# Performance work log

Hardware: AMD Instinct MI355X
Metric: run time of the kernel (lower is better)

## Reference

```python
import jax, jax.numpy as jnp
import numpy as np

T, B, IN, HID, NL = 256, 256, 64, 512, 2
LS = HID // NL  # per-layer hidden size of GRUCellStack


def setup_inputs() -> dict:
    key = jax.random.key(0)
    ks = jax.random.split(key, 9)
    w = lambda k, shape: (jax.random.normal(k, shape, jnp.float32) * 0.05)
    return {
        "obs": jax.random.normal(ks[0], (T, B, IN), jnp.float32),
        "reset": jax.random.randint(ks[1], (T, B), 0, 2).astype(bool),
        "h": jnp.zeros((B, HID), jnp.float32),
        "W_lin": w(ks[2], (HID, IN)),
        "b_lin": jnp.zeros((HID,), jnp.float32),
        "w_ih0": w(ks[3], (3 * LS, HID)),
        "w_hh0": w(ks[4], (3 * LS, LS)),
        "b_ih0": jnp.zeros((3 * LS,), jnp.float32),
        "b_hh0": jnp.zeros((3 * LS,), jnp.float32),
        "w_ih1": w(ks[5], (3 * LS, LS)),
        "w_hh1": w(ks[6], (3 * LS, LS)),
        "b_ih1": jnp.zeros((3 * LS,), jnp.float32),
        "b_hh1": jnp.zeros((3 * LS,), jnp.float32),
    }


def _gru_cell(i_gates, h, w_hh, b_hh):
    # PyTorch nn.GRUCell math; i_gates = x @ w_ih.T + b_ih precomputed.
    h_gates = h @ w_hh.T + b_hh
    ir, iz, in_ = jnp.split(i_gates, 3, axis=-1)
    hr, hz, hn = jnp.split(h_gates, 3, axis=-1)
    r = jax.nn.sigmoid(ir + hr)
    z = jax.nn.sigmoid(iz + hz)
    n = jnp.tanh(in_ + r * hn)
    return (1.0 - z) * n + z * h


def reference(obs, reset, h, W_lin, b_lin, w_ih0, w_hh0, b_ih0, b_hh0,
              w_ih1, w_hh1, b_ih1, b_hh1):
    # embed all timesteps at once: [T,B,HID]
    x = obs.astype(jnp.float32) @ W_lin.T + b_lin
    # layer-0 input-side gates depend only on x -> precompute: [T,B,3*LS]
    ig0 = x @ w_ih0.T + b_ih0
    mask = (~reset).astype(jnp.float32)[..., None]  # [T,B,1]

    def step(hc, inp):
        ig0_t, m_t = inp
        hc = hc * m_t                      # reset masking of full stacked state
        h0, h1 = jnp.split(hc, 2, axis=-1)  # per-layer states [B,LS]
        h0n = _gru_cell(ig0_t, h0, w_hh0, b_hh0)
        ig1 = h0n @ w_ih1.T + b_ih1
        h1n = _gru_cell(ig1, h1, w_hh1, b_hh1)
        hn = jnp.concatenate([h0n, h1n], axis=-1)  # [B,HID]
        return hn, hn

    _, states_h = jax.lax.scan(step, h, (ig0, mask))
    return states_h  # [T,B,HID]
```

## Files before the change

### kernel.cpp

```cpp
#include <hip/hip_runtime.h>

#define T_    256
#define B_    256
#define IN_   64
#define HID_  512
#define LS_   256
#define G3_   768
#define TBS_  16
#define MBT_  128
#define WP_   264
#define FSTRIDE_ 128

typedef short bf16x8v __attribute__((ext_vector_type(8)));
typedef float f32x4  __attribute__((ext_vector_type(4)));
typedef unsigned long long u64;

#define MFMA_B16(A, B, C) __builtin_amdgcn_mfma_f32_16x16x32_bf16(A, B, C, 0, 0, 0)

__device__ __forceinline__ unsigned short f2bf(float f) {
  union { float f; unsigned u; } v; v.f = f;
  unsigned r = v.u + 0x7fffu + ((v.u >> 16) & 1u);
  return (unsigned short)(r >> 16);
}
__device__ __forceinline__ float sigm(float x) { return 1.0f / (1.0f + __expf(-x)); }
__device__ __forceinline__ float tanh_f(float x) {
  x = fminf(fmaxf(x, -15.0f), 15.0f);
  float e = __expf(-2.0f * x);
  return (1.0f - e) / (1.0f + e);
}

__device__ __forceinline__ void st2_coh(unsigned short* p, unsigned short v) {
  __hip_atomic_store(p, v, __ATOMIC_RELAXED, __HIP_MEMORY_SCOPE_AGENT);
}
__device__ __forceinline__ bf16x8v ld16_coh(const unsigned short* p) {
  union { u64 q[2]; bf16x8v v; } u;
  u.q[0] = __hip_atomic_load((const u64*)p,     __ATOMIC_RELAXED, __HIP_MEMORY_SCOPE_AGENT);
  u.q[1] = __hip_atomic_load((const u64*)(p+4), __ATOMIC_RELAXED, __HIP_MEMORY_SCOPE_AGENT);
  return u.v;
}

__global__ void prep_all(const float* __restrict__ whh0, const float* __restrict__ wih1,
                         const float* __restrict__ whh1, const unsigned char* __restrict__ rst,
                         const float* __restrict__ W_lin, const float* __restrict__ b_lin,
                         const float* __restrict__ w_ih0, const float* __restrict__ b_ih0,
                         unsigned short* __restrict__ dst, unsigned short* __restrict__ wc,
                         float* __restrict__ bc, int* __restrict__ flagp,
                         int* __restrict__ flags) {
  const int bx = blockIdx.x;
  const int tid = threadIdx.x;
  if (bx < 1152) {
    const int idx = bx * 512 + tid;
    const int N1 = G3_ * LS_;
    if (idx < 3 * N1) {
      float v;
      if (idx < N1)            v = whh0[idx];
      else if (idx < 2 * N1)   v = wih1[idx - N1];
      else                     v = whh1[idx - 2 * N1];
      dst[idx] = f2bf(v);
    }
    if (bx == 1 && tid < 32) flags[tid * FSTRIDE_] = 0;
    if (bx == 0) {
      __shared__ int f;
      if (tid == 0) f = 0;
      __syncthreads();
      int any = 0;
      for (int i = 0; i < 8; ++i) {
        int off = tid * 8 + i;
        if ((off & 3) && rst[off]) any = 1;
      }
      if (any) atomicOr(&f, 1);
      __syncthreads();
      if (tid == 0) *flagp = f;
    }
  } else {
    const int n = (bx - 1152) * 8 + (tid >> 6);
    const int i = tid & 63;
    const float* wrow = w_ih0 + (size_t)n * HID_;
    float acc = 0.f;
    for (int h = 0; h < HID_; ++h) acc += wrow[h] * W_lin[h * IN_ + i];
    wc[n * IN_ + i] = f2bf(acc);
    float pb = 0.f;
    for (int h = i; h < HID_; h += 64) pb += wrow[h] * b_lin[h];
#pragma unroll
    for (int off = 32; off > 0; off >>= 1) pb += __shfl_down(pb, off);
    if (i == 0) bc[n] = pb + b_ih0[n];
  }
}

__global__ __launch_bounds__(512, 2) void gru_main(
    const float* __restrict__ obs, const unsigned char* __restrict__ rst,
    const float* __restrict__ h_init,
    const unsigned short* __restrict__ wc,
    const unsigned short* __restrict__ whh0g,
    const unsigned short* __restrict__ wih1g, const unsigned short* __restrict__ whh1g,
    const float* __restrict__ bcp, const float* __restrict__ bhh0,
    const float* __restrict__ bih1, const float* __restrict__ bhh1,
    const int* __restrict__ flagp, int* __restrict__ flag0,
    unsigned short* __restrict__ hx0, unsigned short* __restrict__ hx1,
    float* __restrict__ out) {

  __shared__ __align__(16) unsigned short wlds[3 * 96 * WP_];
  __shared__ int s_sm[128];
  __shared__ int s_start_sh;

  const int tid  = threadIdx.x;
  const int lane = tid & 63;
  const int w    = tid >> 6;
  const int l15  = lane & 15;
  const int quad = lane >> 4;

  const int x  = blockIdx.x;
  const int cx = x & 7, m8 = x >> 3;
  const int j  = m8 & 7;
  const int team = cx * 4 + (m8 >> 3);
  const int bg = team & 1, tc = team >> 1;
  const int b0 = bg * MBT_, t0 = tc * TBS_;

  int* f0 = flag0 + team * FSTRIDE_;

  const int flag = *flagp;
#define RVAL(i) (rst[flag ? (i) : ((i) << 2)] != 0)

#pragma unroll
  for (int q = 0; q < 3; ++q) {
    const unsigned short* src = (q == 0) ? whh0g : (q == 1) ? wih1g : whh1g;
    for (int cid = tid; cid < 96 * 32; cid += 512) {
      int lr = cid >> 5, off8 = (cid & 31) * 8;
      int g = lr >> 5, cc = lr & 31;
      int grow = (g << 8) + (j << 5) + cc;
      *(f32x4*)&wlds[(q * 96 + lr) * WP_ + off8] =
          *(const f32x4*)&src[(size_t)grow * 256 + off8];
    }
  }

  float b0r[2], b0z[2], b0i[2], b0h[2], b1r[2], b1z[2], b1i[2], b1h[2];
#pragma unroll
  for (int cg = 0; cg < 2; ++cg) {
    const int c = j * 32 + cg * 16 + l15;
    b0r[cg] = bcp[c] + bhh0[c];
    b0z[cg] = bcp[256 + c] + bhh0[256 + c];
    b0i[cg] = bcp[512 + c];
    b0h[cg] = bhh0[512 + c];
    b1r[cg] = bih1[c] + bhh1[c];
    b1z[cg] = bih1[256 + c] + bhh1[256 + c];
    b1i[cg] = bih1[512 + c];
    b1h[cg] = bhh1[512 + c];
  }

  if (tid < 128) {
    int s = 0;
    for (int tt = t0; tt >= 1; --tt) {
      if (RVAL(tt * B_ + b0 + tid)) { s = tt; break; }
    }
    s_sm[tid] = s;
  }
  __syncthreads();
  if (tid == 0) {
    int s = s_sm[0];
    for (int k = 1; k < 128; ++k) s = s < s_sm[k] ? s : s_sm[k];
    s_start_sh = s;
  }
  __syncthreads();
  const int s_start = s_start_sh;

  bf16x8v h0A[8], h1A[8];
  const bf16x8v z8 = {0, 0, 0, 0, 0, 0, 0, 0};
#pragma unroll
  for (int kc = 0; kc < 8; ++kc) { h0A[kc] = z8; h1A[kc] = z8; }
  float h0v[2][4] = {{0.f}}, h1v[2][4] = {{0.f}};
#pragma unroll
  for (int cg = 0; cg < 2; ++cg)
#pragma unroll
    for (int r = 0; r < 4; ++r) { h0v[cg][r] = 0.f; h1v[cg][r] = 0.f; }
  if (s_start == 0) {
    const float* hrow = h_init + (size_t)(b0 + w * 16 + l15) * HID_;
#pragma unroll
    for (int kc = 0; kc < 8; ++kc) {
      f32x4 u0 = *(const f32x4*)(hrow + kc * 32 + quad * 8);
      f32x4 u1 = *(const f32x4*)(hrow + kc * 32 + quad * 8 + 4);
      f32x4 v0 = *(const f32x4*)(hrow + 256 + kc * 32 + quad * 8);
      f32x4 v1 = *(const f32x4*)(hrow + 256 + kc * 32 + quad * 8 + 4);
      bf16x8v a, b;
#pragma unroll
      for (int e = 0; e < 4; ++e) {
        a[e] = (short)f2bf(u0[e]); a[4 + e] = (short)f2bf(u1[e]);
        b[e] = (short)f2bf(v0[e]); b[4 + e] = (short)f2bf(v1[e]);
      }
      h0A[kc] = a; h1A[kc] = b;
    }
#pragma unroll
    for (int cg = 0; cg < 2; ++cg)
#pragma unroll
      for (int r = 0; r < 4; ++r) {
        const int m = w * 16 + quad * 4 + r;
        const int c = j * 32 + cg * 16 + l15;
        h0v[cg][r] = h_init[(size_t)(b0 + m) * HID_ + c];
        h1v[cg][r] = h_init[(size_t)(b0 + m) * HID_ + 256 + c];
      }
  }

  const unsigned short* wR0 = &wlds[(0 * 96 + 0 * 32 + l15) * WP_];
  const unsigned short* wZ0 = &wlds[(0 * 96 + 1 * 32 + l15) * WP_];
  const unsigned short* wN0 = &wlds[(0 * 96 + 2 * 32 + l15) * WP_];
  const unsigned short* iR1 = &wlds[(1 * 96 + 0 * 32 + l15) * WP_];
  const unsigned short* iZ1 = &wlds[(1 * 96 + 1 * 32 + l15) * WP_];
  const unsigned short* iN1 = &wlds[(1 * 96 + 2 * 32 + l15) * WP_];
  const unsigned short* hR1 = &wlds[(2 * 96 + 0 * 32 + l15) * WP_];
  const unsigned short* hZ1 = &wlds[(2 * 96 + 1 * 32 + l15) * WP_];
  const unsigned short* hN1 = &wlds[(2 * 96 + 2 * 32 + l15) * WP_];
#define CGO_ (16 * WP_)

  f32x4 ou0a, ou0b, ou1a, ou1b;
  {
    const float* po = obs + ((size_t)s_start * B_ + b0 + w * 16 + l15) * IN_;
    ou0a = __builtin_nontemporal_load((const f32x4*)(po + quad * 8));
    ou0b = __builtin_nontemporal_load((const f32x4*)(po + quad * 8 + 4));
    ou1a = __builtin_nontemporal_load((const f32x4*)(po + 32 + quad * 8));
    ou1b = __builtin_nontemporal_load((const f32x4*)(po + 32 + quad * 8 + 4));
  }

  for (int t = s_start; t < t0 + TBS_; ++t) {
    const int  kk = t - s_start + 1;
    const bool wr = (t >= t0);
    const bool rs0 = RVAL(t * B_ + b0 + w * 16 + l15);
    bool rse[4];
#pragma unroll
    for (int r = 0; r < 4; ++r) rse[r] = RVAL(t * B_ + b0 + w * 16 + quad * 4 + r);

    f32x4 ar[2], az[2], ani[2], anh[2];
#pragma unroll
    for (int cg = 0; cg < 2; ++cg) {
      ar[cg] = (f32x4){0.f, 0.f, 0.f, 0.f};
      az[cg] = ar[cg]; ani[cg] = ar[cg]; anh[cg] = ar[cg];
    }
    {
#pragma unroll
      for (int kc = 0; kc < 2; ++kc) {
        f32x4 u0 = kc ? ou1a : ou0a;
        f32x4 u1 = kc ? ou1b : ou0b;
        bf16x8v oA;
#pragma unroll
        for (int e = 0; e < 4; ++e) { oA[e] = (short)f2bf(u0[e]); oA[4 + e] = (short)f2bf(u1[e]); }
#pragma unroll
        for (int cg = 0; cg < 2; ++cg) {
          const size_t wo = (size_t)(j * 32 + cg * 16 + l15) * 64 + kc * 32 + quad * 8;
          bf16x8v br = *(const bf16x8v*)&wc[wo];
          bf16x8v bz = *(const bf16x8v*)&wc[wo + (size_t)256 * 64];
          bf16x8v bn = *(const bf16x8v*)&wc[wo + (size_t)512 * 64];
          ar[cg]  = MFMA_B16(oA, br, ar[cg]);
          az[cg]  = MFMA_B16(oA, bz, az[cg]);
          ani[cg] = MFMA_B16(oA, bn, ani[cg]);
        }
      }
    }
#pragma unroll
    for (int kc = 0; kc < 8; ++kc) {
      bf16x8v am = rs0 ? z8 : h0A[kc];
      const int o = kc * 32 + quad * 8;
#pragma unroll
      for (int cg = 0; cg < 2; ++cg) {
        ar[cg]  = MFMA_B16(am, *(const bf16x8v*)&wR0[o + cg * CGO_], ar[cg]);
        az[cg]  = MFMA_B16(am, *(const bf16x8v*)&wZ0[o + cg * CGO_], az[cg]);
        anh[cg] = MFMA_B16(am, *(const bf16x8v*)&wN0[o + cg * CGO_], anh[cg]);
      }
    }
    {
      unsigned short* hw = hx0 + ((size_t)team * 2 + (kk & 1)) * (MBT_ * 256);
#pragma unroll
      for (int cg = 0; cg < 2; ++cg)
#pragma unroll
        for (int r = 0; r < 4; ++r) {
          const int m = w * 16 + quad * 4 + r;
          float rr = sigm(ar[cg][r] + b0r[cg]);
          float zz = sigm(az[cg][r] + b0z[cg]);
          float nn = tanh_f(ani[cg][r] + b0i[cg] + rr * (anh[cg][r] + b0h[cg]));
          float hp = rse[r] ? 0.f : h0v[cg][r];
          float hv = (1.f - zz) * nn + zz * hp;
          h0v[cg][r] = hv;
          st2_coh(hw + m * 256 + j * 32 + cg * 16 + l15, f2bf(hv));
        }
    }
    __syncthreads();
    if (tid == 0) {
      __hip_atomic_fetch_add(f0, 1, __ATOMIC_RELAXED, __HIP_MEMORY_SCOPE_AGENT);
      int cap = 0;
      while (__hip_atomic_load(f0, __ATOMIC_RELAXED, __HIP_MEMORY_SCOPE_AGENT)
                 < 8 * kk && cap < (1 << 16)) { __builtin_amdgcn_s_sleep(2); ++cap; }
    }
    __syncthreads();
    {
      const unsigned short* hr0 =
          hx0 + ((size_t)team * 2 + (kk & 1)) * (MBT_ * 256) + (w * 16 + l15) * 256;
#pragma unroll
      for (int kc = 0; kc < 8; ++kc)
        h0A[kc] = ld16_coh(hr0 + kc * 32 + quad * 8);
      if (kk >= 2) {
        const unsigned short* hr1 =
            hx1 + ((size_t)team * 2 + ((kk - 1) & 1)) * (MBT_ * 256) + (w * 16 + l15) * 256;
#pragma unroll
        for (int kc = 0; kc < 8; ++kc)
          h1A[kc] = ld16_coh(hr1 + kc * 32 + quad * 8);
      }
    }
    if (wr) {
#pragma unroll
      for (int cg = 0; cg < 2; ++cg)
#pragma unroll
        for (int r = 0; r < 4; ++r) {
          const int m = w * 16 + quad * 4 + r;
          __builtin_nontemporal_store(h0v[cg][r],
              &out[((size_t)t * B_ + b0 + m) * HID_ + j * 32 + cg * 16 + l15]);
        }
    }
    if (t - 1 >= t0) {
#pragma unroll
      for (int cg = 0; cg < 2; ++cg)
#pragma unroll
        for (int r = 0; r < 4; ++r) {
          const int m = w * 16 + quad * 4 + r;
          __builtin_nontemporal_store(h1v[cg][r],
              &out[((size_t)(t - 1) * B_ + b0 + m) * HID_ + 256 + j * 32 + cg * 16 + l15]);
        }
    }
    {
      const int tn = (t + 1 < t0 + TBS_) ? t + 1 : t;
      const float* po = obs + ((size_t)tn * B_ + b0 + w * 16 + l15) * IN_;
      ou0a = __builtin_nontemporal_load((const f32x4*)(po + quad * 8));
      ou0b = __builtin_nontemporal_load((const f32x4*)(po + quad * 8 + 4));
      ou1a = __builtin_nontemporal_load((const f32x4*)(po + 32 + quad * 8));
      ou1b = __builtin_nontemporal_load((const f32x4*)(po + 32 + quad * 8 + 4));
    }

#pragma unroll
    for (int cg = 0; cg < 2; ++cg) {
      ar[cg] = (f32x4){0.f, 0.f, 0.f, 0.f};
      az[cg] = ar[cg]; ani[cg] = ar[cg]; anh[cg] = ar[cg];
    }
#pragma unroll
    for (int kc = 0; kc < 8; ++kc) {
      bf16x8v ai_ = h0A[kc];
      bf16x8v am  = rs0 ? z8 : h1A[kc];
      const int o = kc * 32 + quad * 8;
#pragma unroll
      for (int cg = 0; cg < 2; ++cg) {
        ar[cg]  = MFMA_B16(ai_, *(const bf16x8v*)&iR1[o + cg * CGO_], ar[cg]);
        az[cg]  = MFMA_B16(ai_, *(const bf16x8v*)&iZ1[o + cg * CGO_], az[cg]);
        ani[cg] = MFMA_B16(ai_, *(const bf16x8v*)&iN1[o + cg * CGO_], ani[cg]);
        ar[cg]  = MFMA_B16(am, *(const bf16x8v*)&hR1[o + cg * CGO_], ar[cg]);
        az[cg]  = MFMA_B16(am, *(const bf16x8v*)&hZ1[o + cg * CGO_], az[cg]);
        anh[cg] = MFMA_B16(am, *(const bf16x8v*)&hN1[o + cg * CGO_], anh[cg]);
      }
    }
    {
      unsigned short* hw = hx1 + ((size_t)team * 2 + (kk & 1)) * (MBT_ * 256);
#pragma unroll
      for (int cg = 0; cg < 2; ++cg)
#pragma unroll
        for (int r = 0; r < 4; ++r) {
          const int m = w * 16 + quad * 4 + r;
          float rr = sigm(ar[cg][r] + b1r[cg]);
          float zz = sigm(az[cg][r] + b1z[cg]);
          float nn = tanh_f(ani[cg][r] + b1i[cg] + rr * (anh[cg][r] + b1h[cg]));
          float hp = rse[r] ? 0.f : h1v[cg][r];
          float hv = (1.f - zz) * nn + zz * hp;
          h1v[cg][r] = hv;
          st2_coh(hw + m * 256 + j * 32 + cg * 16 + l15, f2bf(hv));
        }
    }
  }
  {
    const int tl = t0 + TBS_ - 1;
#pragma unroll
    for (int cg = 0; cg < 2; ++cg)
#pragma unroll
      for (int r = 0; r < 4; ++r) {
        const int m = w * 16 + quad * 4 + r;
        __builtin_nontemporal_store(h1v[cg][r],
            &out[((size_t)tl * B_ + b0 + m) * HID_ + 256 + j * 32 + cg * 16 + l15]);
      }
  }
#undef RVAL
#undef CGO_
}

extern "C" void kernel_launch(void* const* d_in, const int* in_sizes, int n_in,
                              void* d_out, int out_size, void* d_ws, size_t ws_size,
                              hipStream_t stream) {
  const float* obs    = (const float*)d_in[0];
  const unsigned char* rst = (const unsigned char*)d_in[1];
  const float* h_init = (const float*)d_in[2];
  const float* W_lin  = (const float*)d_in[3];
  const float* b_lin  = (const float*)d_in[4];
  const float* w_ih0  = (const float*)d_in[5];
  const float* w_hh0  = (const float*)d_in[6];
  const float* b_ih0  = (const float*)d_in[7];
  const float* b_hh0  = (const float*)d_in[8];
  const float* w_ih1  = (const float*)d_in[9];
  const float* w_hh1  = (const float*)d_in[10];
  const float* b_ih1  = (const float*)d_in[11];
  const float* b_hh1  = (const float*)d_in[12];

  char* w = (char*)d_ws;
  unsigned short* wcp   = (unsigned short*)(w);
  unsigned short* whh0b = (unsigned short*)(w + 98304);
  unsigned short* wih1b = (unsigned short*)(w + 491520);
  unsigned short* whh1b = (unsigned short*)(w + 884736);
  float*          bcp   = (float*)(w + 1277952);
  int*            flagp = (int*)(w + 1281024);
  int*            flags = (int*)(w + 1281088);
  unsigned short* hx0   = (unsigned short*)(w + 1310720);
  unsigned short* hx1   = (unsigned short*)(w + 1310720 + 4194304);

  prep_all<<<1152 + 96, 512, 0, stream>>>(w_hh0, w_ih1, w_hh1, rst,
                                          W_lin, b_lin, w_ih0, b_ih0,
                                          whh0b, wcp, bcp, flagp, flags);
  gru_main<<<256, 512, 0, stream>>>(obs, rst, h_init, wcp, whh0b, wih1b, whh1b,
                                    bcp, b_hh0, b_ih1, b_hh1, flagp,
                                    flags, hx0, hx1, (float*)d_out);
}
```

Baseline: 655.4 us.

## Permute K dimension so hidden-state exchange uses packed fragment-ordered stores and loads

Reorders the K index of the recurrent weights in LDS and of the exchanged hidden-state buffers, so each lane stores two bf16 values as one 32-bit atomic instead of two 16-bit stores. The exchange buffer is laid out in MFMA-fragment order so the coherent reloads by each lane hit contiguous 512-byte spans across the wave. The goal is to halve the number of coherent global stores and make the per-step cross-block state exchange better coalesced. The cost is more complex index arithmetic and a K permutation that must stay consistent between the weights, the initial state and the exchanged state.

New measurement: 705.0 us. +7.6%, slower.

```diff
diff --git a/kernel.cpp b/kernel.cpp
--- a/kernel.cpp
+++ b/kernel.cpp
@@ -29,14 +29,18 @@
   return (1.0f - e) / (1.0f + e);
 }
 
-__device__ __forceinline__ void st2_coh(unsigned short* p, unsigned short v) {
-  __hip_atomic_store(p, v, __ATOMIC_RELAXED, __HIP_MEMORY_SCOPE_AGENT);
-}
-__device__ __forceinline__ bf16x8v ld16_coh(const unsigned short* p) {
+__device__ __forceinline__ bf16x8v ld_frag_coh(const char* tb, int w8kc, int l15, int quad) {
+  const char* p = tb + ((size_t)w8kc << 10) + (size_t)((((quad << 4) + l15)) << 3);
   union { u64 q[2]; bf16x8v v; } u;
-  u.q[0] = __hip_atomic_load((const u64*)p,     __ATOMIC_RELAXED, __HIP_MEMORY_SCOPE_AGENT);
-  u.q[1] = __hip_atomic_load((const u64*)(p+4), __ATOMIC_RELAXED, __HIP_MEMORY_SCOPE_AGENT);
+  u.q[0] = __hip_atomic_load((const u64*)p,         __ATOMIC_RELAXED, __HIP_MEMORY_SCOPE_AGENT);
+  u.q[1] = __hip_atomic_load((const u64*)(p + 512), __ATOMIC_RELAXED, __HIP_MEMORY_SCOPE_AGENT);
   return u.v;
+}
+__device__ __forceinline__ void st_pair_coh(char* tb, int m, int j, int l15, unsigned pack) {
+  const int p0 = l15 << 1;
+  char* p = tb + ((size_t)((((m >> 4) << 3) + j)) << 10)
+               + (size_t)(((((p0 >> 3) << 4) + (m & 15)) << 3) + ((p0 & 4) << 7) + ((p0 & 3) << 1));
+  __hip_atomic_store((unsigned*)p, pack, __ATOMIC_RELAXED, __HIP_MEMORY_SCOPE_AGENT);
 }
 
 __global__ void prep_all(const float* __restrict__ whh0, const float* __restrict__ wih1,
@@ -125,11 +129,19 @@
   for (int q = 0; q < 3; ++q) {
     const unsigned short* src = (q == 0) ? whh0g : (q == 1) ? wih1g : whh1g;
     for (int cid = tid; cid < 96 * 32; cid += 512) {
-      int lr = cid >> 5, off8 = (cid & 31) * 8;
+      int lr = cid >> 5, ch = cid & 31;
       int g = lr >> 5, cc = lr & 31;
       int grow = (g << 8) + (j << 5) + cc;
-      *(f32x4*)&wlds[(q * 96 + lr) * WP_ + off8] =
-          *(const f32x4*)&src[(size_t)grow * 256 + off8];
+      int kc = ch >> 2, q4 = (ch & 3) << 2;
+      const unsigned short* s = &src[(size_t)grow * 256 + (kc << 5) + q4];
+      u64 A = *(const u64*)s;
+      u64 B = *(const u64*)(s + 16);
+      u64 o0 = (A & 0xffffull) | ((B & 0xffffull) << 16) |
+               (((A >> 16) & 0xffffull) << 32) | (((B >> 16) & 0xffffull) << 48);
+      u64 o1 = ((A >> 32) & 0xffffull) | (((B >> 32) & 0xffffull) << 16) |
+               (((A >> 48) & 0xffffull) << 32) | (((B >> 48) & 0xffffull) << 48);
+      unsigned short* d = &wlds[(q * 96 + lr) * WP_ + (ch << 3)];
+      *(u64*)d = o0; *((u64*)(d + 4)) = o1;
     }
   }
 
@@ -167,7 +179,7 @@
   const bf16x8v z8 = {0, 0, 0, 0, 0, 0, 0, 0};
 #pragma unroll
   for (int kc = 0; kc < 8; ++kc) { h0A[kc] = z8; h1A[kc] = z8; }
-  float h0v[2][4] = {{0.f}}, h1v[2][4] = {{0.f}};
+  float h0v[2][4], h1v[2][4];
 #pragma unroll
   for (int cg = 0; cg < 2; ++cg)
 #pragma unroll
@@ -176,15 +188,13 @@
     const float* hrow = h_init + (size_t)(b0 + w * 16 + l15) * HID_;
 #pragma unroll
     for (int kc = 0; kc < 8; ++kc) {
-      f32x4 u0 = *(const f32x4*)(hrow + kc * 32 + quad * 8);
-      f32x4 u1 = *(const f32x4*)(hrow + kc * 32 + quad * 8 + 4);
-      f32x4 v0 = *(const f32x4*)(hrow + 256 + kc * 32 + quad * 8);
-      f32x4 v1 = *(const f32x4*)(hrow + 256 + kc * 32 + quad * 8 + 4);
       bf16x8v a, b;
 #pragma unroll
-      for (int e = 0; e < 4; ++e) {
-        a[e] = (short)f2bf(u0[e]); a[4 + e] = (short)f2bf(u1[e]);
-        b[e] = (short)f2bf(v0[e]); b[4 + e] = (short)f2bf(v1[e]);
+      for (int e = 0; e < 8; ++e) {
+        const int p  = (quad << 3) + e;
+        const int lk = ((p & 1) << 4) + (p >> 1);
+        a[e] = (short)f2bf(hrow[(kc << 5) + lk]);
+        b[e] = (short)f2bf(hrow[256 + (kc << 5) + lk]);
       }
       h0A[kc] = a; h1A[kc] = b;
     }
@@ -233,24 +243,22 @@
       ar[cg] = (f32x4){0.f, 0.f, 0.f, 0.f};
       az[cg] = ar[cg]; ani[cg] = ar[cg]; anh[cg] = ar[cg];
     }
-    {
-#pragma unroll
-      for (int kc = 0; kc < 2; ++kc) {
-        f32x4 u0 = kc ? ou1a : ou0a;
-        f32x4 u1 = kc ? ou1b : ou0b;
-        bf16x8v oA;
-#pragma unroll
-        for (int e = 0; e < 4; ++e) { oA[e] = (short)f2bf(u0[e]); oA[4 + e] = (short)f2bf(u1[e]); }
-#pragma unroll
-        for (int cg = 0; cg < 2; ++cg) {
-          const size_t wo = (size_t)(j * 32 + cg * 16 + l15) * 64 + kc * 32 + quad * 8;
-          bf16x8v br = *(const bf16x8v*)&wc[wo];
-          bf16x8v bz = *(const bf16x8v*)&wc[wo + (size_t)256 * 64];
-          bf16x8v bn = *(const bf16x8v*)&wc[wo + (size_t)512 * 64];
-          ar[cg]  = MFMA_B16(oA, br, ar[cg]);
-          az[cg]  = MFMA_B16(oA, bz, az[cg]);
-          ani[cg] = MFMA_B16(oA, bn, ani[cg]);
-        }
+#pragma unroll
+    for (int kc = 0; kc < 2; ++kc) {
+      f32x4 u0 = kc ? ou1a : ou0a;
+      f32x4 u1 = kc ? ou1b : ou0b;
+      bf16x8v oA;
+#pragma unroll
+      for (int e = 0; e < 4; ++e) { oA[e] = (short)f2bf(u0[e]); oA[4 + e] = (short)f2bf(u1[e]); }
+#pragma unroll
+      for (int cg = 0; cg < 2; ++cg) {
+        const size_t wo = (size_t)(j * 32 + cg * 16 + l15) * 64 + kc * 32 + quad * 8;
+        bf16x8v br = *(const bf16x8v*)&wc[wo];
+        bf16x8v bz = *(const bf16x8v*)&wc[wo + (size_t)256 * 64];
+        bf16x8v bn = *(const bf16x8v*)&wc[wo + (size_t)512 * 64];
+        ar[cg]  = MFMA_B16(oA, br, ar[cg]);
+        az[cg]  = MFMA_B16(oA, bz, az[cg]);
+        ani[cg] = MFMA_B16(oA, bn, ani[cg]);
       }
     }
 #pragma unroll
@@ -265,20 +273,23 @@
       }
     }
     {
-      unsigned short* hw = hx0 + ((size_t)team * 2 + (kk & 1)) * (MBT_ * 256);
-#pragma unroll
-      for (int cg = 0; cg < 2; ++cg)
-#pragma unroll
-        for (int r = 0; r < 4; ++r) {
-          const int m = w * 16 + quad * 4 + r;
+      char* tbw = (char*)(hx0 + (size_t)(team * 2 + (kk & 1)) * (MBT_ * 256));
+#pragma unroll
+      for (int r = 0; r < 4; ++r) {
+        const int m = w * 16 + quad * 4 + r;
+        float hvv[2];
+#pragma unroll
+        for (int cg = 0; cg < 2; ++cg) {
           float rr = sigm(ar[cg][r] + b0r[cg]);
           float zz = sigm(az[cg][r] + b0z[cg]);
           float nn = tanh_f(ani[cg][r] + b0i[cg] + rr * (anh[cg][r] + b0h[cg]));
           float hp = rse[r] ? 0.f : h0v[cg][r];
-          float hv = (1.f - zz) * nn + zz * hp;
-          h0v[cg][r] = hv;
-          st2_coh(hw + m * 256 + j * 32 + cg * 16 + l15, f2bf(hv));
+          hvv[cg] = (1.f - zz) * nn + zz * hp;
+          h0v[cg][r] = hvv[cg];
         }
+        st_pair_coh(tbw, m, j, l15,
+                    (unsigned)f2bf(hvv[0]) | ((unsigned)f2bf(hvv[1]) << 16));
+      }
     }
     __syncthreads();
     if (tid == 0) {
@@ -289,17 +300,16 @@
     }
     __syncthreads();
     {
-      const unsigned short* hr0 =
-          hx0 + ((size_t)team * 2 + (kk & 1)) * (MBT_ * 256) + (w * 16 + l15) * 256;
+      const char* tb0 = (const char*)(hx0 + (size_t)(team * 2 + (kk & 1)) * (MBT_ * 256));
 #pragma unroll
       for (int kc = 0; kc < 8; ++kc)
-        h0A[kc] = ld16_coh(hr0 + kc * 32 + quad * 8);
+        h0A[kc] = ld_frag_coh(tb0, w * 8 + kc, l15, quad);
       if (kk >= 2) {
-        const unsigned short* hr1 =
-            hx1 + ((size_t)team * 2 + ((kk - 1) & 1)) * (MBT_ * 256) + (w * 16 + l15) * 256;
+        const char* tb1 =
+            (const char*)(hx1 + (size_t)(team * 2 + ((kk - 1) & 1)) * (MBT_ * 256));
 #pragma unroll
         for (int kc = 0; kc < 8; ++kc)
-          h1A[kc] = ld16_coh(hr1 + kc * 32 + quad * 8);
+          h1A[kc] = ld_frag_coh(tb1, w * 8 + kc, l15, quad);
       }
     }
     if (wr) {
@@ -352,20 +362,23 @@
       }
     }
     {
-      unsigned short* hw = hx1 + ((size_t)team * 2 + (kk & 1)) * (MBT_ * 256);
-#pragma unroll
-      for (int cg = 0; cg < 2; ++cg)
-#pragma unroll
-        for (int r = 0; r < 4; ++r) {
-          const int m = w * 16 + quad * 4 + r;
+      char* tbw = (char*)(hx1 + (size_t)(team * 2 + (kk & 1)) * (MBT_ * 256));
+#pragma unroll
+      for (int r = 0; r < 4; ++r) {
+        const int m = w * 16 + quad * 4 + r;
+        float hvv[2];
+#pragma unroll
+        for (int cg = 0; cg < 2; ++cg) {
           float rr = sigm(ar[cg][r] + b1r[cg]);
           float zz = sigm(az[cg][r] + b1z[cg]);
           float nn = tanh_f(ani[cg][r] + b1i[cg] + rr * (anh[cg][r] + b1h[cg]));
           float hp = rse[r] ? 0.f : h1v[cg][r];
-          float hv = (1.f - zz) * nn + zz * hp;
-          h1v[cg][r] = hv;
-          st2_coh(hw + m * 256 + j * 32 + cg * 16 + l15, f2bf(hv));
+          hvv[cg] = (1.f - zz) * nn + zz * hp;
+          h1v[cg][r] = hvv[cg];
         }
+        st_pair_coh(tbw, m, j, l15,
+                    (unsigned)f2bf(hvv[0]) | ((unsigned)f2bf(hvv[1]) << 16));
+      }
     }
   }
   {
```
